# Performance work log

Hardware: AMD Instinct MI355X
Metric: run time of the kernel (lower is better)

The kernel has to match this reference:

```python
import jax, jax.numpy as jnp
import numpy as np

N_NODES = 50000
N_EDGES = 800000
D = 64
LN_EPS = 1e-5


def setup_inputs() -> dict:
    key = jax.random.key(0)
    k1, k2, k3 = jax.random.split(key, 3)
    x = jax.random.normal(k1, (N_NODES, D), dtype=jnp.float32)
    edge_index = jax.random.randint(k2, (2, N_EDGES), 0, N_NODES, dtype=jnp.int64)
    # GCNConv linear weight (no bias in lin; conv bias separate), kaiming-ish scale
    W = jax.random.normal(k3, (D, D), dtype=jnp.float32) / np.sqrt(D)
    b = jnp.zeros((D,), dtype=jnp.float32)
    # LayerNorm affine params
    gamma = jnp.ones((D,), dtype=jnp.float32)
    beta = jnp.zeros((D,), dtype=jnp.float32)
    return {"x": x, "edge_index": edge_index, "W": W, "b": b, "gamma": gamma, "beta": beta}


def reference(x, edge_index, W, b, gamma, beta):
    n = x.shape[0]
    # --- GCNConv (normalize=True, improved=False, add_self_loops=True) ---
    loops = jnp.arange(n, dtype=edge_index.dtype)
    src = jnp.concatenate([edge_index[0], loops])  # message sources j
    dst = jnp.concatenate([edge_index[1], loops])  # message targets i
    ew = jnp.ones(src.shape[0], dtype=x.dtype)
    deg = jax.ops.segment_sum(ew, dst, num_segments=n)          # in-degree incl. self-loop
    dinv = jnp.where(deg > 0, jax.lax.rsqrt(jnp.where(deg > 0, deg, 1.0)), 0.0)
    norm = dinv[src] * dinv[dst]                                 # [E+N]
    xw = x @ W                                                   # [N, D]
    z = jax.ops.segment_sum(norm[:, None] * xw[src], dst, num_segments=n) + b
    # --- identity skip connection ---
    h = x + z
    # --- norm_act_drop: LayerNorm + ReLU (dropout_prob=0) ---
    mu = jnp.mean(h, axis=-1, keepdims=True)
    var = jnp.mean((h - mu) ** 2, axis=-1, keepdims=True)
    hn = (h - mu) * jax.lax.rsqrt(var + LN_EPS)
    return jax.nn.relu(hn * gamma + beta)
```

## Files before the change

### kernel.cpp

```cpp
#include <hip/hip_runtime.h>
#include <hip/hip_fp16.h>

#define N_NODES 50000
#define N_EDGES 800000
#define D 64
#define LN_EPS 1e-5f
#define CAP 48
#define SENT 50000
#define CNT_PAD 50048
#define XS_ROWS 50008
#define NRG 8
#define RSPAN2 6250
#define NCH2 64
#define CHSZ2 12500
#define HIST_NB (NRG * NCH2)
#define GEMM_NB ((N_NODES + 63) / 64)
#define PREP_NB ((N_EDGES / 4 + 255) / 256)
#define SC_EB 782

typedef unsigned short u16;
typedef unsigned int u32;


__global__ __launch_bounds__(256) void indep_k(const int* __restrict__ src,
                                               const int* __restrict__ dst,
                                               u32* __restrict__ pe,
                                               u16* __restrict__ lpos,
                                               u16* __restrict__ H,
                                               const float* __restrict__ x,
                                               const float* __restrict__ W,
                                               __half* __restrict__ xs) {
    __shared__ u32 smem[RSPAN2];
    int bid = blockIdx.x;
    int tid = threadIdx.x;
    if (bid < HIST_NB) {
        int r = bid & (NRG - 1);
        int c = bid >> 3;
        int lo = r * RSPAN2;
        for (int w = tid; w < RSPAN2; w += 256) smem[w] = 0;
        __syncthreads();
        int cbase = c * CHSZ2;
        for (int i = 0; i < 49; ++i) {
            int e = cbase + i * 256 + tid;
            if (e < cbase + CHSZ2) {
                unsigned tr = (unsigned)dst[e] - (unsigned)lo;
                if (tr < RSPAN2) {
                    u32 old = atomicAdd(&smem[tr], 1u);
                    lpos[e] = (u16)old;
                }
            }
        }
        __syncthreads();
        u32* H32 = (u32*)(H + (size_t)c * N_NODES + lo);
        for (int w = tid; w < RSPAN2 / 2; w += 256)
            H32[w] = (smem[2 * w] & 0xffffu) | (smem[2 * w + 1] << 16);
    } else if (bid < HIST_NB + GEMM_NB) {
        float* xlds = (float*)smem;
        int row0 = (bid - HIST_NB) * 64;
        const float4* xg = (const float4*)(x + (size_t)row0 * D);
        float4* xl4 = (float4*)xlds;
        for (int i = tid; i < D * D / 4; i += 256) {
            int grow = row0 + (i >> 4);
            xl4[i] = (grow < N_NODES) ? xg[i] : make_float4(0.f, 0.f, 0.f, 0.f);
        }
        int lane = tid & 63;
        float wcol[D];
#pragma unroll
        for (int k = 0; k < D; ++k) wcol[k] = W[k * D + lane];
        __syncthreads();
        int wv = tid >> 6;
        for (int rr = 0; rr < 16; ++rr) {
            int rloc = wv * 16 + rr;
            int grow = row0 + rloc;
            if (grow >= N_NODES + 1) break;
            const float4* xr = (const float4*)(xlds + rloc * D);
            float acc = 0.f;
#pragma unroll
            for (int k4 = 0; k4 < 16; ++k4) {
                float4 xv = xr[k4];
                acc += xv.x * wcol[k4 * 4 + 0];
                acc += xv.y * wcol[k4 * 4 + 1];
                acc += xv.z * wcol[k4 * 4 + 2];
                acc += xv.w * wcol[k4 * 4 + 3];
            }
            xs[(size_t)grow * D + lane] = __float2half(acc);
        }
    } else {
        int gid = (bid - HIST_NB - GEMM_NB) * 256 + tid;
        if (gid < N_EDGES / 4) {
            int4 s = ((const int4*)src)[gid];
            int4 d = ((const int4*)dst)[gid];
            uint4 p;
            p.x = (u32)(u16)d.x | ((u32)(u16)s.x << 16);
            p.y = (u32)(u16)d.y | ((u32)(u16)s.y << 16);
            p.z = (u32)(u16)d.z | ((u32)(u16)s.z << 16);
            p.w = (u32)(u16)d.w | ((u32)(u16)s.w << 16);
            ((uint4*)pe)[gid] = p;
        }
    }
}

__global__ __launch_bounds__(256) void pref_scale_k(u16* __restrict__ H,
                                                    int* __restrict__ cnt,
                                                    __half* __restrict__ xs) {
    __shared__ float sdi[256];
    int n0 = blockIdx.x * 256;
    int n = n0 + threadIdx.x;
    bool ok = (n < N_NODES);
    u32 v[NCH2];
#pragma unroll
    for (int c = 0; c < NCH2; ++c)
        v[c] = ok ? (u32)H[(size_t)c * N_NODES + n] : 0;
    u32 run = 0;
#pragma unroll
    for (int c = 0; c < NCH2; ++c) { u32 t = v[c]; v[c] = run; run += t; }
    if (ok) {
#pragma unroll
        for (int c = 0; c < NCH2; ++c)
            H[(size_t)c * N_NODES + n] = (u16)v[c];
        cnt[n] = (int)run;
    }
    sdi[threadIdx.x] = rsqrtf((float)run + 1.0f);
    __syncthreads();
    float4* xs4 = (float4*)xs;
#pragma unroll
    for (int j = 0; j < 8; ++j) {
        int idx = threadIdx.x + j * 256;
        int lrow = idx >> 3;
        int row = n0 + lrow;
        if (row < N_NODES) {
            float di = sdi[lrow];
            size_t g4 = (size_t)row * 8 + (idx & 7);
            float4 raw = xs4[g4];
            __half2* hp = (__half2*)&raw;
#pragma unroll
            for (int i = 0; i < 4; ++i) {
                float2 f = __half22float2(hp[i]);
                hp[i] = __floats2half2_rn(di * f.x, di * f.y);
            }
            xs4[g4] = raw;
        }
    }
}

__global__ __launch_bounds__(256) void scatter_k(const u32* __restrict__ pe,
                                                 const u16* __restrict__ lpos,
                                                 const u16* __restrict__ H,
                                                 u16* __restrict__ ssrc) {
    int e4 = blockIdx.x * 1024 + threadIdx.x * 4;
    if (e4 >= N_EDGES) return;
    uint4 p = ((const uint4*)pe)[e4 >> 2];
    ushort4 lp = ((const ushort4*)lpos)[e4 >> 2];
    int c = e4 / CHSZ2;
    const u16* st = H + (size_t)c * N_NODES;
    u32 pp[4] = {p.x, p.y, p.z, p.w};
    u16 ll[4] = {lp.x, lp.y, lp.z, lp.w};
#pragma unroll
    for (int k = 0; k < 4; ++k) {
        int t = (int)(pp[k] & 0xffffu);
        int pos = (int)st[t] + (int)ll[k];
        if (pos < CAP) ssrc[(size_t)t * CAP + pos] = (u16)(pp[k] >> 16);
    }
}

__global__ __launch_bounds__(256) void agg_ln_k(
        const float* __restrict__ x, const __half* __restrict__ xs,
        const int* __restrict__ cnt, const u16* __restrict__ ssrc,
        const float* __restrict__ b, const float* __restrict__ gamma,
        const float* __restrict__ beta, float* __restrict__ out) {
    int row = blockIdx.x * 4 + (threadIdx.x >> 6);
    if (row >= N_NODES) return;
    int lane = threadIdx.x & 63;
    int sub = lane >> 3;
    int c8  = lane & 7;
    size_t base = (size_t)row * CAP;

    int dc = cnt[row];
    int s0 = ssrc[base + sub + 0];
    int s1 = ssrc[base + sub + 8];
    int s2 = ssrc[base + sub + 16];
    int s3 = ssrc[base + sub + 24];
    int s4 = ssrc[base + sub + 32];
    int s5 = ssrc[base + sub + 40];
    const float4* xp = (const float4*)(x + (size_t)row * D + c8 * 8);
    float4 x0 = xp[0], x1 = xp[1];
    float4 xsr = make_float4(0.f, 0.f, 0.f, 0.f);
    if (sub == 0) xsr = *(const float4*)(xs + (size_t)row * D + c8 * 8);

    int deg = dc < CAP ? dc : CAP;
    int ns = (deg + 7) >> 3;

    int v0 = (sub +  0 < deg) ? s0 : SENT;
    int v1 = (sub +  8 < deg) ? s1 : SENT;
    int v2 = (sub + 16 < deg) ? s2 : SENT;
    int v3 = (sub + 24 < deg) ? s3 : SENT;
    int v4 = (sub + 32 < deg) ? s4 : SENT;
    int v5 = (sub + 40 < deg) ? s5 : SENT;

    float4 r0 = make_float4(0.f,0.f,0.f,0.f), r1 = r0, r2 = r0,
           r3 = r0, r4 = r0, r5 = r0;
    if (0 < ns) r0 = *(const float4*)(xs + (size_t)v0 * D + c8 * 8);
    if (1 < ns) r1 = *(const float4*)(xs + (size_t)v1 * D + c8 * 8);
    if (2 < ns) r2 = *(const float4*)(xs + (size_t)v2 * D + c8 * 8);
    if (3 < ns) r3 = *(const float4*)(xs + (size_t)v3 * D + c8 * 8);
    if (4 < ns) r4 = *(const float4*)(xs + (size_t)v4 * D + c8 * 8);
    if (5 < ns) r5 = *(const float4*)(xs + (size_t)v5 * D + c8 * 8);

    float di = rsqrtf((float)dc + 1.0f);

    float4 a0 = make_float4(0.f, 0.f, 0.f, 0.f);
    float4 a1 = make_float4(0.f, 0.f, 0.f, 0.f);
    {
        float4 rr[7] = {r0, r1, r2, r3, r4, r5, xsr};
#pragma unroll
        for (int k = 0; k < 7; ++k) {
            const __half2* hp = (const __half2*)&rr[k];
            float2 p0 = __half22float2(hp[0]), p1 = __half22float2(hp[1]);
            float2 p2 = __half22float2(hp[2]), p3 = __half22float2(hp[3]);
            a0.x += p0.x; a0.y += p0.y; a0.z += p1.x; a0.w += p1.y;
            a1.x += p2.x; a1.y += p2.y; a1.z += p3.x; a1.w += p3.y;
        }
    }

#pragma unroll
    for (int o = 8; o < 64; o <<= 1) {
        a0.x += __shfl_xor(a0.x, o, 64); a0.y += __shfl_xor(a0.y, o, 64);
        a0.z += __shfl_xor(a0.z, o, 64); a0.w += __shfl_xor(a0.w, o, 64);
        a1.x += __shfl_xor(a1.x, o, 64); a1.y += __shfl_xor(a1.y, o, 64);
        a1.z += __shfl_xor(a1.z, o, 64); a1.w += __shfl_xor(a1.w, o, 64);
    }

    const float4* bp = (const float4*)(b + c8 * 8);
    float4 b0 = bp[0], b1 = bp[1];

    float h[8];
    h[0] = x0.x + di * a0.x + b0.x;
    h[1] = x0.y + di * a0.y + b0.y;
    h[2] = x0.z + di * a0.z + b0.z;
    h[3] = x0.w + di * a0.w + b0.w;
    h[4] = x1.x + di * a1.x + b1.x;
    h[5] = x1.y + di * a1.y + b1.y;
    h[6] = x1.z + di * a1.z + b1.z;
    h[7] = x1.w + di * a1.w + b1.w;

    float s_ = 0.f;
#pragma unroll
    for (int i = 0; i < 8; ++i) s_ += h[i];
#pragma unroll
    for (int o = 1; o < 64; o <<= 1) s_ += __shfl_xor(s_, o, 64);
    float mu = s_ * (1.0f / 512.0f);
    float v_ = 0.f;
    float dd[8];
#pragma unroll
    for (int i = 0; i < 8; ++i) { dd[i] = h[i] - mu; v_ += dd[i] * dd[i]; }
#pragma unroll
    for (int o = 1; o < 64; o <<= 1) v_ += __shfl_xor(v_, o, 64);
    float rstd = rsqrtf(v_ * (1.0f / 512.0f) + LN_EPS);

    if (sub == 0) {
        const float4* gp = (const float4*)(gamma + c8 * 8);
        const float4* ep = (const float4*)(beta + c8 * 8);
        float4 g0 = gp[0], g1 = gp[1];
        float4 e0 = ep[0], e1 = ep[1];
        float4 w0, w1;
        w0.x = fmaxf(dd[0] * rstd * g0.x + e0.x, 0.f);
        w0.y = fmaxf(dd[1] * rstd * g0.y + e0.y, 0.f);
        w0.z = fmaxf(dd[2] * rstd * g0.z + e0.z, 0.f);
        w0.w = fmaxf(dd[3] * rstd * g0.w + e0.w, 0.f);
        w1.x = fmaxf(dd[4] * rstd * g1.x + e1.x, 0.f);
        w1.y = fmaxf(dd[5] * rstd * g1.y + e1.y, 0.f);
        w1.z = fmaxf(dd[6] * rstd * g1.z + e1.z, 0.f);
        w1.w = fmaxf(dd[7] * rstd * g1.w + e1.w, 0.f);
        float4* op = (float4*)(out + (size_t)row * D + c8 * 8);
        op[0] = w0;
        op[1] = w1;
    }
}

extern "C" void kernel_launch(void* const* d_in, const int* in_sizes, int n_in,
                              void* d_out, int out_size, void* d_ws, size_t ws_size,
                              hipStream_t stream) {
    const float* x     = (const float*)d_in[0];
    const int*   ei    = (const int*)d_in[1];
    const float* W     = (const float*)d_in[2];
    const float* b     = (const float*)d_in[3];
    const float* gamma = (const float*)d_in[4];
    const float* beta  = (const float*)d_in[5];
    float* out = (float*)d_out;

    const int* src = ei;
    const int* dst = ei + N_EDGES;

    int*    cnt  = (int*)d_ws;
    __half* xs   = (__half*)(cnt + CNT_PAD);
    u32*    pe   = (u32*)(xs + (size_t)XS_ROWS * D);
    u16*    H    = (u16*)(pe + N_EDGES);
    u16*    lpos = H + (size_t)NCH2 * N_NODES;
    u16*    ssrc = lpos + N_EDGES;

    indep_k<<<HIST_NB + GEMM_NB + PREP_NB, 256, 0, stream>>>(
        src, dst, pe, lpos, H, x, W, xs);
    pref_scale_k<<<(N_NODES + 255) / 256, 256, 0, stream>>>(H, cnt, xs);
    scatter_k<<<SC_EB, 256, 0, stream>>>(pe, lpos, H, ssrc);
    agg_ln_k<<<(N_NODES + 3) / 4, 256, 0, stream>>>(x, xs, cnt, ssrc, b, gamma, beta, out);
}
```

Before: 163.0 us.

## Drop packed edge buffer, pack histogram as u16 pairs, vectorize dst loads

Removes the prep stage that packed src/dst into a 32-bit edge array. The scatter kernel now reads the raw int32 src/dst arrays directly, which saves one write and one read pass over a workspace buffer and some block launches. The histogram blocks now pack two 16-bit counters per shared-memory word, halving LDS footprint and initialization, and read dst with int4 vector loads. The trade-off is that scatter reads twice as many bytes for edges, and packed-counter atomics could interfere if a per-node count overflowed 16 bits.

```diff
diff --git a/kernel.cpp b/kernel.cpp
--- a/kernel.cpp
+++ b/kernel.cpp
@@ -15,46 +15,52 @@
 #define CHSZ2 12500
 #define HIST_NB (NRG * NCH2)
 #define GEMM_NB ((N_NODES + 63) / 64)
-#define PREP_NB ((N_EDGES / 4 + 255) / 256)
 #define SC_EB 782
 
 typedef unsigned short u16;
 typedef unsigned int u32;
 
 
-__global__ __launch_bounds__(256) void indep_k(const int* __restrict__ src,
-                                               const int* __restrict__ dst,
-                                               u32* __restrict__ pe,
+__global__ __launch_bounds__(256) void indep_k(const int* __restrict__ dst,
                                                u16* __restrict__ lpos,
                                                u16* __restrict__ H,
                                                const float* __restrict__ x,
                                                const float* __restrict__ W,
                                                __half* __restrict__ xs) {
-    __shared__ u32 smem[RSPAN2];
+    __shared__ u32 smem[4096];
     int bid = blockIdx.x;
     int tid = threadIdx.x;
     if (bid < HIST_NB) {
         int r = bid & (NRG - 1);
         int c = bid >> 3;
         int lo = r * RSPAN2;
-        for (int w = tid; w < RSPAN2; w += 256) smem[w] = 0;
+        for (int w = tid; w < RSPAN2 / 2; w += 256) smem[w] = 0;
         __syncthreads();
         int cbase = c * CHSZ2;
-        for (int i = 0; i < 49; ++i) {
-            int e = cbase + i * 256 + tid;
-            if (e < cbase + CHSZ2) {
-                unsigned tr = (unsigned)dst[e] - (unsigned)lo;
-                if (tr < RSPAN2) {
-                    u32 old = atomicAdd(&smem[tr], 1u);
-                    lpos[e] = (u16)old;
+        const int4* d4 = (const int4*)(dst + cbase);
+#pragma unroll
+        for (int i = 0; i < 13; ++i) {
+            int g = i * 256 + tid;
+            if (g < CHSZ2 / 4) {
+                int4 dv = d4[g];
+                int e = cbase + g * 4;
+                int dd[4] = {dv.x, dv.y, dv.z, dv.w};
+#pragma unroll
+                for (int k = 0; k < 4; ++k) {
+                    unsigned tr = (unsigned)dd[k] - (unsigned)lo;
+                    if (tr < RSPAN2) {
+                        u32 addend = (tr & 1) ? 0x10000u : 1u;
+                        u32 old = atomicAdd(&smem[tr >> 1], addend);
+                        lpos[e + k] = (u16)((tr & 1) ? (old >> 16) : (old & 0xffffu));
+                    }
                 }
             }
         }
         __syncthreads();
         u32* H32 = (u32*)(H + (size_t)c * N_NODES + lo);
         for (int w = tid; w < RSPAN2 / 2; w += 256)
-            H32[w] = (smem[2 * w] & 0xffffu) | (smem[2 * w + 1] << 16);
-    } else if (bid < HIST_NB + GEMM_NB) {
+            H32[w] = smem[w];
+    } else {
         float* xlds = (float*)smem;
         int row0 = (bid - HIST_NB) * 64;
         const float4* xg = (const float4*)(x + (size_t)row0 * D);
@@ -85,18 +91,6 @@
             }
             xs[(size_t)grow * D + lane] = __float2half(acc);
         }
-    } else {
-        int gid = (bid - HIST_NB - GEMM_NB) * 256 + tid;
-        if (gid < N_EDGES / 4) {
-            int4 s = ((const int4*)src)[gid];
-            int4 d = ((const int4*)dst)[gid];
-            uint4 p;
-            p.x = (u32)(u16)d.x | ((u32)(u16)s.x << 16);
-            p.y = (u32)(u16)d.y | ((u32)(u16)s.y << 16);
-            p.z = (u32)(u16)d.z | ((u32)(u16)s.z << 16);
-            p.w = (u32)(u16)d.w | ((u32)(u16)s.w << 16);
-            ((uint4*)pe)[gid] = p;
-        }
     }
 }
 
@@ -143,23 +137,26 @@
     }
 }
 
-__global__ __launch_bounds__(256) void scatter_k(const u32* __restrict__ pe,
+__global__ __launch_bounds__(256) void scatter_k(const int* __restrict__ src,
+                                                 const int* __restrict__ dst,
                                                  const u16* __restrict__ lpos,
                                                  const u16* __restrict__ H,
                                                  u16* __restrict__ ssrc) {
     int e4 = blockIdx.x * 1024 + threadIdx.x * 4;
     if (e4 >= N_EDGES) return;
-    uint4 p = ((const uint4*)pe)[e4 >> 2];
+    int4 dv = ((const int4*)dst)[e4 >> 2];
+    int4 sv = ((const int4*)src)[e4 >> 2];
     ushort4 lp = ((const ushort4*)lpos)[e4 >> 2];
     int c = e4 / CHSZ2;
     const u16* st = H + (size_t)c * N_NODES;
-    u32 pp[4] = {p.x, p.y, p.z, p.w};
+    int td[4] = {dv.x, dv.y, dv.z, dv.w};
+    int ts[4] = {sv.x, sv.y, sv.z, sv.w};
     u16 ll[4] = {lp.x, lp.y, lp.z, lp.w};
 #pragma unroll
     for (int k = 0; k < 4; ++k) {
-        int t = (int)(pp[k] & 0xffffu);
+        int t = td[k];
         int pos = (int)st[t] + (int)ll[k];
-        if (pos < CAP) ssrc[(size_t)t * CAP + pos] = (u16)(pp[k] >> 16);
+        if (pos < CAP) ssrc[(size_t)t * CAP + pos] = (u16)ts[k];
     }
 }
 
@@ -293,14 +290,12 @@
 
     int*    cnt  = (int*)d_ws;
     __half* xs   = (__half*)(cnt + CNT_PAD);
-    u32*    pe   = (u32*)(xs + (size_t)XS_ROWS * D);
-    u16*    H    = (u16*)(pe + N_EDGES);
+    u16*    H    = (u16*)(xs + (size_t)XS_ROWS * D);
     u16*    lpos = H + (size_t)NCH2 * N_NODES;
     u16*    ssrc = lpos + N_EDGES;
 
-    indep_k<<<HIST_NB + GEMM_NB + PREP_NB, 256, 0, stream>>>(
-        src, dst, pe, lpos, H, x, W, xs);
+    indep_k<<<HIST_NB + GEMM_NB, 256, 0, stream>>>(dst, lpos, H, x, W, xs);
     pref_scale_k<<<(N_NODES + 255) / 256, 256, 0, stream>>>(H, cnt, xs);
-    scatter_k<<<SC_EB, 256, 0, stream>>>(pe, lpos, H, ssrc);
+    scatter_k<<<SC_EB, 256, 0, stream>>>(src, dst, lpos, H, ssrc);
     agg_ln_k<<<(N_NODES + 3) / 4, 256, 0, stream>>>(x, xs, cnt, ssrc, b, gamma, beta, out);
 }
```

Measured after the change: 154.2 us. 5.4% less time.
